# Performance work log

Hardware: AMD Instinct MI355X
Metric: run time of the kernel (lower is better)

Reference implementation:

```python
import jax, jax.numpy as jnp
import numpy as np

DIM = 512

def setup_inputs() -> dict:
    key = jax.random.key(0)
    ks = jax.random.split(key, 10)
    B, N, D = 8, 4096, DIM
    s = 1.0 / np.sqrt(D)
    return {
        "x": jax.random.normal(ks[0], (B, N, D), dtype=jnp.float32),
        "wq": jax.random.normal(ks[1], (D, D), dtype=jnp.float32) * s,
        "bq": jnp.zeros((D,), dtype=jnp.float32),
        "wk": jax.random.normal(ks[2], (D, D), dtype=jnp.float32) * s,
        "bk": jnp.zeros((D,), dtype=jnp.float32),
        "wp": jax.random.normal(ks[3], (D, D), dtype=jnp.float32) * s,
        "bp": jnp.zeros((D,), dtype=jnp.float32),
        "wf": jax.random.normal(ks[4], (D, D), dtype=jnp.float32) * s,
        "bf": jnp.zeros((D,), dtype=jnp.float32),
        "w_g": jax.random.normal(ks[5], (D, 1), dtype=jnp.float32),
    }

def reference(x, wq, bq, wk, bk, wp, bp, wf, bf, w_g):
    D = x.shape[-1]
    scale = D ** (-0.5)
    query = x @ wq + bq                      # [B,N,D]
    key_t = x @ wk + bk                      # [B,N,D]
    # l2 normalize along last dim (tf.math.l2_normalize uses eps=1e-12 via rsqrt of max(sum_sq, eps))
    def l2n(t):
        ss = jnp.sum(t * t, axis=-1, keepdims=True)
        return t * jax.lax.rsqrt(jnp.maximum(ss, 1e-12))
    query = l2n(query)
    key_t = l2n(key_t)
    query_weight = query @ w_g               # [B,N,1]
    scaled = query_weight * scale
    # Faithful to TF code: softmax over axis=-1 of a size-1 axis -> all ones
    attn = jax.nn.softmax(scaled, axis=-1)   # [B,N,1] == 1.0
    global_queries = jnp.sum(attn * query, axis=1)  # [B,D]
    gq = global_queries[:, None, :]          # broadcast over N (tile)
    out = (gq * key_t) @ wp + bp + query     # [B,N,D]
    out = out @ wf + bf
    return out
```

## Files before the change

### kernel.cpp

```cpp
#include <hip/hip_runtime.h>
#include <stdint.h>

typedef __bf16 bf16x8 __attribute__((ext_vector_type(8)));
typedef float floatx4 __attribute__((ext_vector_type(4)));
typedef unsigned short u16;
typedef u16 u16x8 __attribute__((ext_vector_type(8)));

__device__ __forceinline__ float bf2f(u16 u) {
    union { uint32_t i; float f; } v; v.i = ((uint32_t)u) << 16; return v.f;
}
__device__ __forceinline__ u16 f2bf(float f) {
    union { float f; uint32_t i; } v; v.f = f;
    uint32_t r = v.i + 0x7fffu + ((v.i >> 16) & 1u);
    return (u16)(r >> 16);
}

__device__ __forceinline__ void gload_lds16(const u16* g, u16* l) {
    __builtin_amdgcn_global_load_lds(
        (const __attribute__((address_space(1))) void*)g,
        (__attribute__((address_space(3))) void*)l,
        16, 0, 0);
}

#define TM 128
#define TN 128
#define BK 64
#define RSTR 132
#define FSTR 132

template<int EPI>
__global__ __launch_bounds__(256) void gemm_bt(
    const u16* __restrict__ A, int lda,
    const u16* __restrict__ Bt, long bstride,
    const float* __restrict__ bias,
    const u16* __restrict__ addsrc, int ldadd,
    const float* __restrict__ ssq_add,
    const float* __restrict__ ssq_row,
    float* __restrict__ ssq_out,
    u16* __restrict__ C16, float* __restrict__ C32, int ldc,
    int K)
{
    __shared__ __attribute__((aligned(16))) u16 lds[TM * RSTR];
    u16* lsA = lds;
    u16* lsB = lds + TM * BK;
    const int tid  = threadIdx.x;
    const int wave = tid >> 6;
    const int lane = tid & 63;
    const int quad = lane >> 4;
    const int l16  = lane & 15;
    const int wm = wave >> 1, wn = wave & 1;

    const int gx   = gridDim.x;
    const int nwg  = gx * gridDim.y;
    const int wgid = blockIdx.y * gx + blockIdx.x;
    const int cpx  = nwg >> 3;
    const int swz  = (wgid & 7) * cpx + (wgid >> 3);
    const int row0 = (swz / gx) * TM;
    const int col0 = (swz % gx) * TN;
    const int batch = row0 >> 12;
    const int Mtot  = gridDim.y * TM;

    floatx4 acc[4][4] = {};

    const int rsub = lane >> 3;
    const int ksub = ((lane & 7) ^ rsub) << 3;
    const u16* aptr[4]; const u16* bptr[4];
    const u16* Bb = Bt + (size_t)batch * bstride;
#pragma unroll
    for (int c = 0; c < 4; ++c) {
        const int cc = wave * 4 + c;
        aptr[c] = A  + (size_t)(row0 + cc * 8 + rsub) * lda + ksub;
        bptr[c] = Bb + (size_t)(col0 + cc * 8 + rsub) * K   + ksub;
    }

    for (int kt = 0; kt < K; kt += BK) {
#pragma unroll
        for (int c = 0; c < 4; ++c) {
            const int cc = wave * 4 + c;
            gload_lds16(aptr[c] + kt, &lsA[cc * 512]);
            gload_lds16(bptr[c] + kt, &lsB[cc * 512]);
        }
        __syncthreads();
#pragma unroll
        for (int ks = 0; ks < 2; ++ks) {
            const int cidx = ks * 4 + quad;
            const int pgo = ((cidx ^ (l16 & 7)) << 3);
            bf16x8 af[4], bfr[4];
#pragma unroll
            for (int i = 0; i < 4; ++i) {
                int m = wm * 64 + i * 16 + l16;
                af[i] = *(const bf16x8*)&lsA[m * BK + pgo];
            }
#pragma unroll
            for (int j = 0; j < 4; ++j) {
                int n = wn * 64 + j * 16 + l16;
                bfr[j] = *(const bf16x8*)&lsB[n * BK + pgo];
            }
#pragma unroll
            for (int i = 0; i < 4; ++i)
#pragma unroll
                for (int j = 0; j < 4; ++j)
                    acc[i][j] = __builtin_amdgcn_mfma_f32_16x16x32_bf16(af[i], bfr[j], acc[i][j], 0, 0, 0);
        }
        __syncthreads();
    }

    if constexpr (EPI == 0 || EPI == 1) {
        float rsr[16], rsa[16];
        if constexpr (EPI == 1) {
#pragma unroll
            for (int i = 0; i < 4; ++i)
#pragma unroll
                for (int t = 0; t < 4; ++t) {
                    int rowb = row0 + wm * 64 + i * 16 + quad * 4 + t;
                    rsr[i * 4 + t] = rsqrtf(fmaxf(ssq_row[rowb], 1e-12f));
                    rsa[i * 4 + t] = rsqrtf(fmaxf(ssq_add[rowb], 1e-12f));
                }
        }
#pragma unroll
        for (int j = 0; j < 4; ++j) {
            int col = col0 + wn * 64 + j * 16 + l16;
            float bv = bias[col];
            int tcol = wn * 64 + j * 16 + l16;
#pragma unroll
            for (int i = 0; i < 4; ++i) {
                int trow = wm * 64 + i * 16 + quad * 4;
                int rowb = row0 + trow;
#pragma unroll
                for (int t = 0; t < 4; ++t) {
                    float v;
                    if constexpr (EPI == 1) {
                        v = acc[i][j][t] * rsr[i * 4 + t] + bv
                          + bf2f(addsrc[(size_t)(rowb + t) * ldadd + col]) * rsa[i * 4 + t];
                    } else {
                        v = acc[i][j][t] + bv;
                        (void)rowb;
                    }
                    lds[(trow + t) * RSTR + tcol] = f2bf(v);
                }
            }
        }
        __syncthreads();
        float ssl[8];
#pragma unroll
        for (int c = 0; c < 8; ++c) {
            int r  = c * 16 + (tid >> 4);
            int cu = (tid & 15) * 8;
            ushort4 lo = *(const ushort4*)&lds[r * RSTR + cu];
            ushort4 hi = *(const ushort4*)&lds[r * RSTR + cu + 4];
            u16x8 o;
            o[0] = lo.x; o[1] = lo.y; o[2] = lo.z; o[3] = lo.w;
            o[4] = hi.x; o[5] = hi.y; o[6] = hi.z; o[7] = hi.w;
            *(u16x8*)&C16[(size_t)(row0 + r) * ldc + col0 + cu] = o;
            if constexpr (EPI == 0) {
                float ss = 0.f;
#pragma unroll
                for (int q2 = 0; q2 < 8; ++q2) { float f = bf2f(o[q2]); ss += f * f; }
                ssl[c] = ss;
            }
        }
        if constexpr (EPI == 0) {
            float* so = ssq_out + (size_t)(col0 >> 9) * Mtot + row0;
#pragma unroll
            for (int c = 0; c < 8; ++c) {
                float s = ssl[c];
                s += __shfl_xor(s, 1);
                s += __shfl_xor(s, 2);
                s += __shfl_xor(s, 4);
                s += __shfl_xor(s, 8);
                if ((lane & 15) == 0) atomicAdd(&so[c * 16 + (tid >> 4)], s);
            }
        }
    } else {
        float* ftile = (float*)lds;
#pragma unroll
        for (int pass = 0; pass < 2; ++pass) {
            __syncthreads();
            if (wm == pass) {
#pragma unroll
                for (int j = 0; j < 4; ++j) {
                    int tcol = wn * 64 + j * 16 + l16;
                    float bv = bias[col0 + tcol];
#pragma unroll
                    for (int i = 0; i < 4; ++i) {
                        int trow = i * 16 + quad * 4;
#pragma unroll
                        for (int t = 0; t < 4; ++t)
                            ftile[(trow + t) * FSTR + tcol] = acc[i][j][t] + bv;
                    }
                }
            }
            __syncthreads();
#pragma unroll
            for (int c = 0; c < 8; ++c) {
                int r  = c * 8 + (tid >> 5);
                int cu = (tid & 31) * 4;
                float4 v = *(const float4*)&ftile[r * FSTR + cu];
                *(float4*)&C32[(size_t)(row0 + pass * 64 + r) * ldc + col0 + cu] = v;
            }
        }
    }
}

__global__ __launch_bounds__(256) void gsum_kernel(const u16* __restrict__ QK,
                                                   const float* __restrict__ ssqQ,
                                                   float* __restrict__ g)
{
    __shared__ float gtile[4][512];
    const int lane = threadIdx.x & 63;
    const int wave = threadIdx.x >> 6;
    const int row0 = blockIdx.x * 128 + wave * 32;
    const int batch = row0 >> 12;
    const int d = lane * 8;
    float gacc[8] = {};
    for (int rr = 0; rr < 32; ++rr) {
        int row = row0 + rr;
        float s = rsqrtf(fmaxf(ssqQ[row], 1e-12f));
        u16x8 q = *(const u16x8*)(QK + (size_t)row * 1024 + d);
#pragma unroll
        for (int i = 0; i < 8; ++i) gacc[i] += s * bf2f(q[i]);
    }
#pragma unroll
    for (int i = 0; i < 8; ++i) gtile[wave][d + i] = gacc[i];
    __syncthreads();
    int c2 = threadIdx.x * 2;
    float s0 = gtile[0][c2]     + gtile[1][c2]     + gtile[2][c2]     + gtile[3][c2];
    float s1 = gtile[0][c2 + 1] + gtile[1][c2 + 1] + gtile[2][c2 + 1] + gtile[3][c2 + 1];
    atomicAdd(&g[batch * 512 + c2], s0);
    atomicAdd(&g[batch * 512 + c2 + 1], s1);
}

__global__ __launch_bounds__(256) void scale_wp_kernel(const float* __restrict__ wp,
                                                       const float* __restrict__ g,
                                                       u16* __restrict__ BtP8)
{
    __shared__ u16 tile[32][34];
    const int b   = blockIdx.x >> 8;
    const int bid = blockIdx.x & 255;
    const int tk = bid & 15;
    const int tn = bid >> 4;
    const int c  = threadIdx.x & 31;
    const int r0 = threadIdx.x >> 5;
    const float* gb = g + b * 512;
#pragma unroll
    for (int i = 0; i < 4; ++i) {
        int r = r0 + i * 8;
        int k = tk * 32 + r;
        tile[r][c] = f2bf(gb[k] * wp[(size_t)k * 512 + tn * 32 + c]);
    }
    __syncthreads();
    u16* Bt = BtP8 + (size_t)b * 512 * 512;
#pragma unroll
    for (int i = 0; i < 4; ++i) {
        int r = r0 + i * 8;
        Bt[(size_t)(tn * 32 + r) * 512 + tk * 32 + c] = tile[c][r];
    }
}

__global__ __launch_bounds__(256) void convert_x_kernel(const float* __restrict__ x, u16* __restrict__ xb)
{
    size_t i = ((size_t)blockIdx.x * 256 + threadIdx.x) * 4;
    float4 v = *(const float4*)(x + i);
    ushort4 o;
    o.x = f2bf(v.x); o.y = f2bf(v.y); o.z = f2bf(v.z); o.w = f2bf(v.w);
    *(ushort4*)(xb + i) = o;
}

__global__ __launch_bounds__(256) void transpose3_kernel(
    const float* __restrict__ w0, const float* __restrict__ w1, const float* __restrict__ w2,
    u16* __restrict__ d0, u16* __restrict__ d1, u16* __restrict__ d2)
{
    __shared__ u16 tile[32][34];
    const int which = blockIdx.x >> 8;
    const float* W = (which == 0) ? w0 : (which == 1) ? w1 : w2;
    u16* Bt = (which == 0) ? d0 : (which == 1) ? d1 : d2;
    const int bid = blockIdx.x & 255;
    const int tk = bid & 15;
    const int tn = bid >> 4;
    const int c  = threadIdx.x & 31;
    const int r0 = threadIdx.x >> 5;
#pragma unroll
    for (int i = 0; i < 4; ++i) {
        int r = r0 + i * 8;
        tile[r][c] = f2bf(W[(size_t)(tk * 32 + r) * 512 + tn * 32 + c]);
    }
    __syncthreads();
#pragma unroll
    for (int i = 0; i < 4; ++i) {
        int r = r0 + i * 8;
        Bt[(size_t)(tn * 32 + r) * 512 + tk * 32 + c] = tile[c][r];
    }
}

__global__ __launch_bounds__(256) void setup_kernel(const float* __restrict__ bq,
                                                    const float* __restrict__ bk,
                                                    float* __restrict__ biasQK,
                                                    float* __restrict__ g,
                                                    float* __restrict__ ssq)
{
    int id = blockIdx.x * 256 + threadIdx.x;
    if (id < 1024) biasQK[id] = (id < 512) ? bq[id] : bk[id - 512];
    if (id < 4096) g[id] = 0.f;
    ssq[id] = 0.f;
}

extern "C" void kernel_launch(void* const* d_in, const int* in_sizes, int n_in,
                              void* d_out, int out_size, void* d_ws, size_t ws_size,
                              hipStream_t stream)
{
    const float* x  = (const float*)d_in[0];
    const float* wq = (const float*)d_in[1];
    const float* bq = (const float*)d_in[2];
    const float* wk = (const float*)d_in[3];
    const float* bk = (const float*)d_in[4];
    const float* wp = (const float*)d_in[5];
    const float* bp = (const float*)d_in[6];
    const float* wf = (const float*)d_in[7];
    const float* bf = (const float*)d_in[8];

    char* ws = (char*)d_ws;
    u16*   xb     = (u16*)(ws);
    u16*   T      = (u16*)(ws);
    u16*   QK     = (u16*)(ws + 33554432);
    u16*   Bt1    = (u16*)(ws + 100663296);
    u16*   BtP8   = (u16*)(ws + 101711872);
    u16*   BtF    = (u16*)(ws + 105906176);
    float* biasQK = (float*)(ws + 106430464);
    float* g      = (float*)(ws + 106434560);
    float* ssq    = (float*)(ws + 106450944);

    setup_kernel<<<256, 256, 0, stream>>>(bq, bk, biasQK, g, ssq);
    convert_x_kernel<<<16384, 256, 0, stream>>>(x, xb);
    transpose3_kernel<<<768, 256, 0, stream>>>(wq, wk, wf, Bt1, Bt1 + 512 * 512, BtF);

    gemm_bt<0><<<dim3(8, 256), 256, 0, stream>>>(
        xb, 512, Bt1, 0, biasQK, nullptr, 0, nullptr, nullptr, ssq, QK, nullptr, 1024, 512);
    gsum_kernel<<<256, 256, 0, stream>>>(QK, ssq, g);
    scale_wp_kernel<<<2048, 256, 0, stream>>>(wp, g, BtP8);
    gemm_bt<1><<<dim3(4, 256), 256, 0, stream>>>(
        QK + 512, 1024, BtP8, 512 * 512, bp, QK, 1024, ssq, ssq + 32768, nullptr, T, nullptr, 512, 512);
    gemm_bt<2><<<dim3(4, 256), 256, 0, stream>>>(
        T, 512, BtF, 0, bf, nullptr, 0, nullptr, nullptr, nullptr, nullptr, (float*)d_out, 512, 512);
}
```

Before: 261.5 us.

## Enlarge GEMM tiles to 256x256 with 8 waves and double-buffered LDS prefetch

The bf16 GEMM kernel moves from 128x128 tiles with 4 waves to 256x256 tiles with 8 waves (512 threads). It adds a two-stage LDS double buffer that uses global_load_lds prefetch with explicit vmcnt waits and raw barriers, and raises wave priority around the MFMA block. The epilogues are reworked to write the larger tile in halves or quarters. The aim is more operand reuse per loaded byte and overlap of global loads with MFMA work. The cost is 128KB of LDS per block, fewer blocks overall (512 for QK, 256 for the others), and more register pressure.

```diff
diff --git a/kernel.cpp b/kernel.cpp
--- a/kernel.cpp
+++ b/kernel.cpp
@@ -22,14 +22,9 @@
         16, 0, 0);
 }
 
-#define TM 128
-#define TN 128
 #define BK 64
-#define RSTR 132
-#define FSTR 132
-
 template<int EPI>
-__global__ __launch_bounds__(256) void gemm_bt(
+__global__ __launch_bounds__(512, 2) void gemm_bt(
     const u16* __restrict__ A, int lda,
     const u16* __restrict__ Bt, long bstride,
     const float* __restrict__ bias,
@@ -40,27 +35,25 @@
     u16* __restrict__ C16, float* __restrict__ C32, int ldc,
     int K)
 {
-    __shared__ __attribute__((aligned(16))) u16 lds[TM * RSTR];
-    u16* lsA = lds;
-    u16* lsB = lds + TM * BK;
+    __shared__ __attribute__((aligned(16))) u16 lds[2 * 32768];
     const int tid  = threadIdx.x;
     const int wave = tid >> 6;
     const int lane = tid & 63;
     const int quad = lane >> 4;
     const int l16  = lane & 15;
-    const int wm = wave >> 1, wn = wave & 1;
+    const int wm = wave >> 2, wn = wave & 3;
 
     const int gx   = gridDim.x;
     const int nwg  = gx * gridDim.y;
     const int wgid = blockIdx.y * gx + blockIdx.x;
     const int cpx  = nwg >> 3;
     const int swz  = (wgid & 7) * cpx + (wgid >> 3);
-    const int row0 = (swz / gx) * TM;
-    const int col0 = (swz % gx) * TN;
+    const int row0 = (swz / gx) * 256;
+    const int col0 = (swz % gx) * 256;
     const int batch = row0 >> 12;
-    const int Mtot  = gridDim.y * TM;
-
-    floatx4 acc[4][4] = {};
+    const int Mtot  = gridDim.y * 256;
+
+    floatx4 acc[8][4] = {};
 
     const int rsub = lane >> 3;
     const int ksub = ((lane & 7) ^ rsub) << 3;
@@ -73,130 +66,164 @@
         bptr[c] = Bb + (size_t)(col0 + cc * 8 + rsub) * K   + ksub;
     }
 
-    for (int kt = 0; kt < K; kt += BK) {
-#pragma unroll
-        for (int c = 0; c < 4; ++c) {
-            const int cc = wave * 4 + c;
-            gload_lds16(aptr[c] + kt, &lsA[cc * 512]);
-            gload_lds16(bptr[c] + kt, &lsB[cc * 512]);
-        }
-        __syncthreads();
+    const int NT = K >> 6;
+
+#define STAGE(T, B)                                                        \
+    {                                                                      \
+        u16* sA_ = &lds[(B) * 32768];                                      \
+        u16* sB_ = sA_ + 16384;                                            \
+        const int kt_ = (T) * BK;                                          \
+        _Pragma("unroll")                                                  \
+        for (int c = 0; c < 4; ++c) {                                      \
+            const int cc = wave * 4 + c;                                   \
+            gload_lds16(aptr[c] + kt_, &sA_[cc * 512]);                    \
+            gload_lds16(bptr[c] + kt_, &sB_[cc * 512]);                    \
+        }                                                                  \
+    }
+
+    STAGE(0, 0);
+    STAGE(1, 1);
+
+    for (int t = 0; t < NT; ++t) {
+        if (t + 1 < NT) asm volatile("s_waitcnt vmcnt(8)" ::: "memory");
+        else            asm volatile("s_waitcnt vmcnt(0)" ::: "memory");
+        __builtin_amdgcn_s_barrier();
+        __builtin_amdgcn_sched_barrier(0);
+
+        const u16* sA = &lds[(t & 1) * 32768];
+        const u16* sB = sA + 16384;
 #pragma unroll
         for (int ks = 0; ks < 2; ++ks) {
             const int cidx = ks * 4 + quad;
             const int pgo = ((cidx ^ (l16 & 7)) << 3);
-            bf16x8 af[4], bfr[4];
-#pragma unroll
-            for (int i = 0; i < 4; ++i) {
-                int m = wm * 64 + i * 16 + l16;
-                af[i] = *(const bf16x8*)&lsA[m * BK + pgo];
-            }
-#pragma unroll
-            for (int j = 0; j < 4; ++j) {
-                int n = wn * 64 + j * 16 + l16;
-                bfr[j] = *(const bf16x8*)&lsB[n * BK + pgo];
-            }
-#pragma unroll
-            for (int i = 0; i < 4; ++i)
-#pragma unroll
-                for (int j = 0; j < 4; ++j)
-                    acc[i][j] = __builtin_amdgcn_mfma_f32_16x16x32_bf16(af[i], bfr[j], acc[i][j], 0, 0, 0);
+            bf16x8 bfr[4];
+#pragma unroll
+            for (int n = 0; n < 4; ++n)
+                bfr[n] = *(const bf16x8*)&sB[(wn * 64 + n * 16 + l16) * BK + pgo];
+            __builtin_amdgcn_s_setprio(1);
+#pragma unroll
+            for (int m = 0; m < 8; ++m) {
+                bf16x8 af = *(const bf16x8*)&sA[(wm * 128 + m * 16 + l16) * BK + pgo];
+#pragma unroll
+                for (int n = 0; n < 4; ++n)
+                    acc[m][n] = __builtin_amdgcn_mfma_f32_16x16x32_bf16(af, bfr[n], acc[m][n], 0, 0, 0);
+            }
+            __builtin_amdgcn_s_setprio(0);
         }
-        __syncthreads();
-    }
+
+        __builtin_amdgcn_sched_barrier(0);
+        asm volatile("" ::: "memory");
+        __builtin_amdgcn_s_barrier();
+        asm volatile("" ::: "memory");
+        if (t + 2 < NT) STAGE(t + 2, t & 1);
+    }
+#undef STAGE
 
     if constexpr (EPI == 0 || EPI == 1) {
-        float rsr[16], rsa[16];
-        if constexpr (EPI == 1) {
-#pragma unroll
-            for (int i = 0; i < 4; ++i)
-#pragma unroll
-                for (int t = 0; t < 4; ++t) {
-                    int rowb = row0 + wm * 64 + i * 16 + quad * 4 + t;
-                    rsr[i * 4 + t] = rsqrtf(fmaxf(ssq_row[rowb], 1e-12f));
-                    rsa[i * 4 + t] = rsqrtf(fmaxf(ssq_add[rowb], 1e-12f));
+        u16* til = lds;
+#pragma unroll
+        for (int h = 0; h < 2; ++h) {
+            __syncthreads();
+            if (wm == h) {
+                float bv[4];
+#pragma unroll
+                for (int n = 0; n < 4; ++n) bv[n] = bias[col0 + wn * 64 + n * 16 + l16];
+#pragma unroll
+                for (int m = 0; m < 8; ++m) {
+                    int rowl = m * 16 + quad * 4;
+                    int rowb = row0 + h * 128 + rowl;
+                    float rsr4[4], rsa4[4];
+                    if constexpr (EPI == 1) {
+                        float4 rr = *(const float4*)&ssq_row[rowb];
+                        float4 ra = *(const float4*)&ssq_add[rowb];
+                        rsr4[0] = rsqrtf(fmaxf(rr.x, 1e-12f));
+                        rsr4[1] = rsqrtf(fmaxf(rr.y, 1e-12f));
+                        rsr4[2] = rsqrtf(fmaxf(rr.z, 1e-12f));
+                        rsr4[3] = rsqrtf(fmaxf(rr.w, 1e-12f));
+                        rsa4[0] = rsqrtf(fmaxf(ra.x, 1e-12f));
+                        rsa4[1] = rsqrtf(fmaxf(ra.y, 1e-12f));
+                        rsa4[2] = rsqrtf(fmaxf(ra.z, 1e-12f));
+                        rsa4[3] = rsqrtf(fmaxf(ra.w, 1e-12f));
+                    }
+#pragma unroll
+                    for (int n = 0; n < 4; ++n) {
+                        int tcol = wn * 64 + n * 16 + l16;
+#pragma unroll
+                        for (int t = 0; t < 4; ++t) {
+                            float v;
+                            if constexpr (EPI == 1) {
+                                v = acc[m][n][t] * rsr4[t] + bv[n]
+                                  + bf2f(addsrc[(size_t)(rowb + t) * ldadd + col0 + tcol]) * rsa4[t];
+                            } else {
+                                v = acc[m][n][t] + bv[n];
+                            }
+                            til[(rowl + t) * 264 + tcol] = f2bf(v);
+                        }
+                    }
                 }
-        }
-#pragma unroll
-        for (int j = 0; j < 4; ++j) {
-            int col = col0 + wn * 64 + j * 16 + l16;
-            float bv = bias[col];
-            int tcol = wn * 64 + j * 16 + l16;
-#pragma unroll
-            for (int i = 0; i < 4; ++i) {
-                int trow = wm * 64 + i * 16 + quad * 4;
-                int rowb = row0 + trow;
-#pragma unroll
-                for (int t = 0; t < 4; ++t) {
-                    float v;
-                    if constexpr (EPI == 1) {
-                        v = acc[i][j][t] * rsr[i * 4 + t] + bv
-                          + bf2f(addsrc[(size_t)(rowb + t) * ldadd + col]) * rsa[i * 4 + t];
-                    } else {
-                        v = acc[i][j][t] + bv;
-                        (void)rowb;
-                    }
-                    lds[(trow + t) * RSTR + tcol] = f2bf(v);
+            }
+            __syncthreads();
+            float ssl[8];
+#pragma unroll
+            for (int c = 0; c < 8; ++c) {
+                int r  = c * 16 + (tid >> 5);
+                int cu = (tid & 31) * 8;
+                ushort4 lo = *(const ushort4*)&til[r * 264 + cu];
+                ushort4 hi = *(const ushort4*)&til[r * 264 + cu + 4];
+                u16x8 o;
+                o[0] = lo.x; o[1] = lo.y; o[2] = lo.z; o[3] = lo.w;
+                o[4] = hi.x; o[5] = hi.y; o[6] = hi.z; o[7] = hi.w;
+                *(u16x8*)&C16[(size_t)(row0 + h * 128 + r) * ldc + col0 + cu] = o;
+                if constexpr (EPI == 0) {
+                    float ss = 0.f;
+#pragma unroll
+                    for (int q2 = 0; q2 < 8; ++q2) { float f = bf2f(o[q2]); ss += f * f; }
+                    ssl[c] = ss;
                 }
             }
-        }
-        __syncthreads();
-        float ssl[8];
-#pragma unroll
-        for (int c = 0; c < 8; ++c) {
-            int r  = c * 16 + (tid >> 4);
-            int cu = (tid & 15) * 8;
-            ushort4 lo = *(const ushort4*)&lds[r * RSTR + cu];
-            ushort4 hi = *(const ushort4*)&lds[r * RSTR + cu + 4];
-            u16x8 o;
-            o[0] = lo.x; o[1] = lo.y; o[2] = lo.z; o[3] = lo.w;
-            o[4] = hi.x; o[5] = hi.y; o[6] = hi.z; o[7] = hi.w;
-            *(u16x8*)&C16[(size_t)(row0 + r) * ldc + col0 + cu] = o;
             if constexpr (EPI == 0) {
-                float ss = 0.f;
-#pragma unroll
-                for (int q2 = 0; q2 < 8; ++q2) { float f = bf2f(o[q2]); ss += f * f; }
-                ssl[c] = ss;
-            }
-        }
-        if constexpr (EPI == 0) {
-            float* so = ssq_out + (size_t)(col0 >> 9) * Mtot + row0;
-#pragma unroll
-            for (int c = 0; c < 8; ++c) {
-                float s = ssl[c];
-                s += __shfl_xor(s, 1);
-                s += __shfl_xor(s, 2);
-                s += __shfl_xor(s, 4);
-                s += __shfl_xor(s, 8);
-                if ((lane & 15) == 0) atomicAdd(&so[c * 16 + (tid >> 4)], s);
+                float* so = ssq_out + (size_t)(col0 >> 9) * Mtot + row0 + h * 128;
+#pragma unroll
+                for (int c = 0; c < 8; ++c) {
+                    float s = ssl[c];
+                    s += __shfl_xor(s, 1);
+                    s += __shfl_xor(s, 2);
+                    s += __shfl_xor(s, 4);
+                    s += __shfl_xor(s, 8);
+                    s += __shfl_xor(s, 16);
+                    if ((lane & 31) == 0) atomicAdd(&so[c * 16 + (tid >> 5)], s);
+                }
             }
         }
     } else {
         float* ftile = (float*)lds;
 #pragma unroll
-        for (int pass = 0; pass < 2; ++pass) {
+        for (int p = 0; p < 4; ++p) {
             __syncthreads();
-            if (wm == pass) {
-#pragma unroll
-                for (int j = 0; j < 4; ++j) {
-                    int tcol = wn * 64 + j * 16 + l16;
-                    float bv = bias[col0 + tcol];
-#pragma unroll
-                    for (int i = 0; i < 4; ++i) {
-                        int trow = i * 16 + quad * 4;
+            if (wm == (p >> 1)) {
+                float bv[4];
+#pragma unroll
+                for (int n = 0; n < 4; ++n) bv[n] = bias[col0 + wn * 64 + n * 16 + l16];
+#pragma unroll
+                for (int mi = 0; mi < 4; ++mi) {
+                    int m = (p & 1) * 4 + mi;
+                    int rowl = mi * 16 + quad * 4;
+#pragma unroll
+                    for (int n = 0; n < 4; ++n) {
+                        int tcol = wn * 64 + n * 16 + l16;
 #pragma unroll
                         for (int t = 0; t < 4; ++t)
-                            ftile[(trow + t) * FSTR + tcol] = acc[i][j][t] + bv;
+                            ftile[(rowl + t) * 264 + tcol] = acc[m][n][t] + bv[n];
                     }
                 }
             }
             __syncthreads();
 #pragma unroll
             for (int c = 0; c < 8; ++c) {
-                int r  = c * 8 + (tid >> 5);
-                int cu = (tid & 31) * 4;
-                float4 v = *(const float4*)&ftile[r * FSTR + cu];
-                *(float4*)&C32[(size_t)(row0 + pass * 64 + r) * ldc + col0 + cu] = v;
+                int r  = c * 8 + wave;
+                int cu = lane * 4;
+                float4 v = *(const float4*)&ftile[r * 264 + cu];
+                *(float4*)&C32[(size_t)(row0 + p * 64 + r) * ldc + col0 + cu] = v;
             }
         }
     }
@@ -333,12 +360,12 @@
     convert_x_kernel<<<16384, 256, 0, stream>>>(x, xb);
     transpose3_kernel<<<768, 256, 0, stream>>>(wq, wk, wf, Bt1, Bt1 + 512 * 512, BtF);
 
-    gemm_bt<0><<<dim3(8, 256), 256, 0, stream>>>(
+    gemm_bt<0><<<dim3(4, 128), 512, 0, stream>>>(
         xb, 512, Bt1, 0, biasQK, nullptr, 0, nullptr, nullptr, ssq, QK, nullptr, 1024, 512);
     gsum_kernel<<<256, 256, 0, stream>>>(QK, ssq, g);
     scale_wp_kernel<<<2048, 256, 0, stream>>>(wp, g, BtP8);
-    gemm_bt<1><<<dim3(4, 256), 256, 0, stream>>>(
+    gemm_bt<1><<<dim3(2, 128), 512, 0, stream>>>(
         QK + 512, 1024, BtP8, 512 * 512, bp, QK, 1024, ssq, ssq + 32768, nullptr, T, nullptr, 512, 512);
-    gemm_bt<2><<<dim3(4, 256), 256, 0, stream>>>(
+    gemm_bt<2><<<dim3(2, 128), 512, 0, stream>>>(
         T, 512, BtF, 0, bf, nullptr, 0, nullptr, nullptr, nullptr, nullptr, (float*)d_out, 512, 512);
 }
```

New measurement: 254.8 us. 2.6% less time.
